# Performance work log

Measured on AMD Instinct MI355X. Metric: run time of the kernel, lower is better.

## Reference

```python
import jax, jax.numpy as jnp
from jax import lax
import numpy as np


def _edt_to(zero_mask):
    """Exact Euclidean distance from every pixel to the nearest True pixel of
    zero_mask. Equivalent to scipy.ndimage.distance_transform_edt(~zero_mask).
    Separable two-pass algorithm: 1-D distance along W (two scans), then an
    exact lower-envelope min along H using squared distances.
    zero_mask: bool [B, H, W] -> float32 [B, H, W].
    """
    B, H, W = zero_mask.shape
    INF = jnp.float32(H + W)  # larger than any attainable 1-D distance
    bg = jnp.transpose(zero_mask, (2, 0, 1))  # [W, B, H]: scan over W

    def step(c, b):
        c = jnp.where(b, 0.0, c + 1.0)
        return c, c

    init = jnp.full((B, H), INF, dtype=jnp.float32)
    _, f = lax.scan(step, init, bg)                 # left-to-right
    _, r = lax.scan(step, init, bg, reverse=True)   # right-to-left
    d1 = jnp.minimum(f, r)                          # [W, B, H] 1-D dist along W
    g = jnp.transpose(d1 * d1, (1, 2, 0))           # [B, H, W] squared 1-D dist

    # d2[b, y, x] = min_{y'} g[b, y', x] + (y - y')^2   (exact 2-D squared EDT)
    yy = jnp.arange(H, dtype=jnp.float32)
    dy2 = (yy[:, None] - yy[None, :]) ** 2          # [H, H']
    d2 = jnp.min(g[:, None, :, :] + dy2[None, :, :, None], axis=2)  # [B, H, W]
    return jnp.sqrt(d2)


def _boundary_loss(preds, targets, idx_class=None):
    B, C, H, W = preds.shape
    probs = jax.nn.softmax(preds, axis=1)
    classes = [idx_class] if idx_class is not None else list(range(1, C))
    total = jnp.float32(0.0)
    count = jnp.float32(0.0)
    for cls in classes:
        pos = targets == cls        # bool [B, H, W]
        neg = ~pos
        has = jnp.any(pos)
        # scipy: distance(negmask)*negmask - (distance(posmask)-1)*posmask
        # distance_transform_edt(negmask) == dist to nearest pos pixel, etc.
        dmap = _edt_to(pos) * neg - (_edt_to(neg) - 1.0) * pos
        loss = jnp.mean(dmap * probs[:, cls])
        total = total + jnp.where(has, loss, 0.0)
        count = count + has.astype(jnp.float32)
    return jnp.where(count > 0, total / jnp.maximum(count, 1.0), jnp.float32(0.0))


def setup_inputs() -> dict:
    key = jax.random.key(0)
    k1, k2 = jax.random.split(key)
    preds = jax.random.normal(k1, (8, 4, 256, 256), dtype=jnp.float32)
    targets = jax.random.randint(k2, (8, 256, 256), 0, 4)
    return {"preds": preds, "targets": targets}


def reference(preds, targets):
    return _boundary_loss(preds, targets, idx_class=None)
```

## Files before the change

kernel.cpp:

```cpp
#include <hip/hip_runtime.h>
#include <math.h>

#define BB 8
#define HH 256
#define WW 256
#define T  2
#define NW 4
#define PAD 96
#define LDSW (WW + 2 * PAD)

typedef unsigned long long u64;

__global__ __launch_bounds__(128) void build_masks(const int* __restrict__ tgt,
                                                   unsigned short* __restrict__ masks16,
                                                   float* __restrict__ out) {
  const int tx = threadIdx.x;
  const int xh = blockIdx.x & 1;
  const int b  = blockIdx.x >> 1;
  const int w  = blockIdx.y;
  const int q  = blockIdx.z;
  const int x  = xh * 128 + tx;
  if (b == 0 && w == 0 && q == 0 && x == 0) out[0] = 0.0f;
  unsigned m0 = 0, m1 = 0, m2 = 0, m3 = 0, bit = 1u;
  const int* p = tgt + ((size_t)b * HH + w * 64 + q * 16) * WW + x;
  for (int r = 0; r < 16; ++r, bit += bit) {
    int e = p[r * WW];
    m0 |= (e == 0) ? bit : 0u;
    m1 |= (e == 1) ? bit : 0u;
    m2 |= (e == 2) ? bit : 0u;
    m3 |= (e == 3) ? bit : 0u;
  }
  unsigned short* mp = masks16 + (((size_t)(b * NW + w) * WW + x) * 4) * 4 + q;
  mp[0]  = (unsigned short)m0;
  mp[4]  = (unsigned short)m1;
  mp[8]  = (unsigned short)m2;
  mp[12] = (unsigned short)m3;
}

__global__ __launch_bounds__(256, 4) void fused(const u64* __restrict__ masks,
                                                const float* __restrict__ preds,
                                                float* __restrict__ out) {
  __shared__ float g[T][LDSW][4];
  __shared__ float fred[4];
  const int x  = threadIdx.x;
  const int b  = blockIdx.x;
  const int y0 = blockIdx.y * T;
  const int wy = y0 >> 6;

  u64 m[NW][4];
  {
    const u64* mb = masks + ((size_t)b * NW * WW + x) * 4;
#pragma unroll
    for (int w = 0; w < NW; ++w) {
      ulonglong2 lo = *(const ulonglong2*)(mb + (size_t)w * WW * 4 + 0);
      ulonglong2 hi = *(const ulonglong2*)(mb + (size_t)w * WW * 4 + 2);
      m[w][0] = lo.x; m[w][1] = lo.y; m[w][2] = hi.x; m[w][3] = hi.y;
    }
  }

  float pr[T][4];
#pragma unroll
  for (int j = 0; j < T; ++j) {
    const float* pb = preds + ((size_t)b * 4 * HH + (y0 + j)) * WW + x;
    pr[j][0] = pb[0 * HH * WW];
    pr[j][1] = pb[1 * HH * WW];
    pr[j][2] = pb[2 * HH * WW];
    pr[j][3] = pb[3 * HH * WW];
  }

  for (int i = x; i < T * 2 * PAD; i += 256) {
    int j = i / (2 * PAD);
    int q = i - j * (2 * PAD);
    int idx = (q < PAD) ? q : (q + WW);
    *(float4*)&g[j][idx][0] = make_float4(1e30f, 1e30f, 1e30f, 1e30f);
  }

  float d[T][4];
  int lmax = 0;
#pragma unroll
  for (int j = 0; j < T; ++j) {
    const int y  = y0 + j;
    const int ly = y & 63;
    const int ini = min(513 + y, 768 - y);
    float4 gv;
    float* gp = (float*)&gv;
#pragma unroll
    for (int k = 0; k < 4; ++k) {
      int best = ini;
#pragma unroll
      for (int w = 0; w < NW; ++w) {
        u64 bits = m[w][k];
        if (w < wy) {
          int dd = y - (w * 64 + 63 - __clzll((long long)bits));
          best = min(best, bits ? dd : 1024);
        } else if (w > wy) {
          int dd = w * 64 + (__ffsll((long long)bits) - 1) - y;
          best = min(best, bits ? dd : 1024);
        } else {
          u64 lo = bits & ((2ull << ly) - 1ull);
          u64 hi = bits >> ly;
          int dl = ly - 63 + __clzll((long long)lo);
          int dh = __ffsll((long long)hi) - 1;
          best = min(best, lo ? dl : 1024);
          best = min(best, hi ? dh : 1024);
        }
      }
      lmax = max(lmax, best);
      gp[k] = (float)(best * best);
      d[j][k] = gp[k];
    }
    *(float4*)&g[j][x + PAD][0] = gv;
  }

#pragma unroll
  for (int off = 32; off; off >>= 1) lmax = max(lmax, __shfl_xor(lmax, off, 64));
  const int R  = __builtin_amdgcn_readfirstlane(lmax);
  const int Rw = min(R, PAD);
  __syncthreads();

  bool alldone = false;
  for (int kk = 1; kk <= Rw; ++kk) {
    float fkk = (float)kk;
    float fk2 = fkk * fkk;
    float dmax = 0.0f;
#pragma unroll
    for (int j = 0; j < T; ++j) {
      float4 gm = *(const float4*)&g[j][x + PAD - kk][0];
      float4 gp = *(const float4*)&g[j][x + PAD + kk][0];
      d[j][0] = fminf(d[j][0], fminf(gm.x, gp.x) + fk2);
      d[j][1] = fminf(d[j][1], fminf(gm.y, gp.y) + fk2);
      d[j][2] = fminf(d[j][2], fminf(gm.z, gp.z) + fk2);
      d[j][3] = fminf(d[j][3], fminf(gm.w, gp.w) + fk2);
      dmax = fmaxf(dmax, fmaxf(fmaxf(d[j][0], d[j][1]), fmaxf(d[j][2], d[j][3])));
    }
    if (__all(dmax <= fk2)) { alldone = true; break; }
  }
  if (!alldone && R > PAD) {
#pragma unroll 1
    for (int kk = PAD + 1; kk <= R; ++kk) {
      int xm = max(x - kk, 0), xp = min(x + kk, WW - 1);
      float dm = (float)(x - xm), dpq = (float)(xp - x);
      float dm2 = dm * dm, dp2 = dpq * dpq;
      float dmax = 0.0f;
#pragma unroll
      for (int j = 0; j < T; ++j) {
        float4 gm = *(const float4*)&g[j][xm + PAD][0];
        float4 gp = *(const float4*)&g[j][xp + PAD][0];
        d[j][0] = fminf(d[j][0], fminf(gm.x + dm2, gp.x + dp2));
        d[j][1] = fminf(d[j][1], fminf(gm.y + dm2, gp.y + dp2));
        d[j][2] = fminf(d[j][2], fminf(gm.z + dm2, gp.z + dp2));
        d[j][3] = fminf(d[j][3], fminf(gm.w + dm2, gp.w + dp2));
        dmax = fmaxf(dmax, fmaxf(fmaxf(d[j][0], d[j][1]), fmaxf(d[j][2], d[j][3])));
      }
      float fkk = (float)kk;
      if (__all(dmax <= fkk * fkk)) break;
    }
  }

  float acc = 0.0f;
#pragma unroll
  for (int j = 0; j < T; ++j) {
    const int ly = (y0 + j) & 63;
    const int t = (int)((m[wy][1] >> ly) & 1ull) * 1 +
                  (int)((m[wy][2] >> ly) & 1ull) * 2 +
                  (int)((m[wy][3] >> ly) & 1ull) * 3;
    float p0 = pr[j][0], p1 = pr[j][1], p2 = pr[j][2], p3 = pr[j][3];
    float pm = fmaxf(fmaxf(p0, p1), fmaxf(p2, p3));
    float e0 = expf(p0 - pm), e1 = expf(p1 - pm);
    float e2 = expf(p2 - pm), e3 = expf(p3 - pm);
    float inv = 1.0f / (e0 + e1 + e2 + e3);

    float dn1 = fminf(d[j][0], fminf(d[j][2], d[j][3]));
    float dn2 = fminf(d[j][0], fminf(d[j][1], d[j][3]));
    float dn3 = fminf(d[j][0], fminf(d[j][1], d[j][2]));
    float c1 = (t == 1) ? (1.0f - sqrtf(dn1)) : sqrtf(d[j][1]);
    float c2 = (t == 2) ? (1.0f - sqrtf(dn2)) : sqrtf(d[j][2]);
    float c3 = (t == 3) ? (1.0f - sqrtf(dn3)) : sqrtf(d[j][3]);
    acc += (c1 * e1 + c2 * e2 + c3 * e3) * inv;
  }

#pragma unroll
  for (int off = 32; off; off >>= 1) acc += __shfl_down(acc, off, 64);
  if ((x & 63) == 0) fred[x >> 6] = acc;
  __syncthreads();
  if (x == 0)
    atomicAdd(out, (fred[0] + fred[1] + fred[2] + fred[3]) *
                       (1.0f / (3.0f * BB * HH * WW)));
}

extern "C" void kernel_launch(void* const* d_in, const int* in_sizes, int n_in,
                              void* d_out, int out_size, void* d_ws, size_t ws_size,
                              hipStream_t stream) {
  const float* preds = (const float*)d_in[0];
  const int*   tgt   = (const int*)d_in[1];
  float* out   = (float*)d_out;
  u64*   masks = (u64*)d_ws;

  build_masks<<<dim3(BB * 2, NW, 4), 128, 0, stream>>>(tgt, (unsigned short*)masks, out);
  fused<<<dim3(BB, HH / T), 256, 0, stream>>>(masks, preds, out);
}
```

Before: 79.76 us.

## Process four rows per block, hoist cross-window column scans, mask finished lanes

Doubles rows per block (T=2→4) and lowers the occupancy hint so each block amortises the mask loads and the per-column scan of the other 64-row windows. The nearest-set-bit positions in the other windows are computed once per column instead of once per row. The horizontal lower-envelope loop now skips the LDS reads for lanes whose current distances are already final, keeping a per-lane done flag. The costs are half as many blocks, higher register and LDS use per block, and extra divergent branches in the inner loop.

```diff
diff --git a/kernel.cpp b/kernel.cpp
--- a/kernel.cpp
+++ b/kernel.cpp
@@ -4,7 +4,7 @@
 #define BB 8
 #define HH 256
 #define WW 256
-#define T  2
+#define T  4
 #define NW 4
 #define PAD 96
 #define LDSW (WW + 2 * PAD)
@@ -37,7 +37,7 @@
   mp[12] = (unsigned short)m3;
 }
 
-__global__ __launch_bounds__(256, 4) void fused(const u64* __restrict__ masks,
+__global__ __launch_bounds__(256, 2) void fused(const u64* __restrict__ masks,
                                                 const float* __restrict__ preds,
                                                 float* __restrict__ out) {
   __shared__ float g[T][LDSW][4];
@@ -75,6 +75,27 @@
     *(float4*)&g[j][idx][0] = make_float4(1e30f, 1e30f, 1e30f, 1e30f);
   }
 
+  int posmax[4] = {-4096, -4096, -4096, -4096};
+  int posmin[4] = { 8192,  8192,  8192,  8192};
+#pragma unroll
+  for (int w = 0; w < NW; ++w) {
+    if (w < wy) {
+#pragma unroll
+      for (int k = 0; k < 4; ++k) {
+        u64 bits = m[w][k];
+        int pos = w * 64 + 63 - __clzll((long long)bits);
+        posmax[k] = max(posmax[k], bits ? pos : -4096);
+      }
+    } else if (w > wy) {
+#pragma unroll
+      for (int k = 0; k < 4; ++k) {
+        u64 bits = m[w][k];
+        int pos = w * 64 + (__ffsll((long long)bits) - 1);
+        posmin[k] = min(posmin[k], bits ? pos : 8192);
+      }
+    }
+  }
+
   float d[T][4];
   int lmax = 0;
 #pragma unroll
@@ -83,31 +104,22 @@
     const int ly = y & 63;
     const int ini = min(513 + y, 768 - y);
     float4 gv;
-    float* gp = (float*)&gv;
+    float* gp_ = (float*)&gv;
 #pragma unroll
     for (int k = 0; k < 4; ++k) {
-      int best = ini;
-#pragma unroll
-      for (int w = 0; w < NW; ++w) {
-        u64 bits = m[w][k];
-        if (w < wy) {
-          int dd = y - (w * 64 + 63 - __clzll((long long)bits));
-          best = min(best, bits ? dd : 1024);
-        } else if (w > wy) {
-          int dd = w * 64 + (__ffsll((long long)bits) - 1) - y;
-          best = min(best, bits ? dd : 1024);
-        } else {
-          u64 lo = bits & ((2ull << ly) - 1ull);
-          u64 hi = bits >> ly;
-          int dl = ly - 63 + __clzll((long long)lo);
-          int dh = __ffsll((long long)hi) - 1;
-          best = min(best, lo ? dl : 1024);
-          best = min(best, hi ? dh : 1024);
-        }
-      }
+      u64 bits = m[wy][k];
+      u64 lo = bits & ((2ull << ly) - 1ull);
+      u64 hi = bits >> ly;
+      int dl = ly - 63 + __clzll((long long)lo);
+      int dh = __ffsll((long long)hi) - 1;
+      int best = min(ini, y - posmax[k]);
+      best = min(best, posmin[k] - y);
+      best = min(best, lo ? dl : 1024);
+      best = min(best, hi ? dh : 1024);
       lmax = max(lmax, best);
-      gp[k] = (float)(best * best);
-      d[j][k] = gp[k];
+      float fb = (float)(best * best);
+      gp_[k] = fb;
+      d[j][k] = fb;
     }
     *(float4*)&g[j][x + PAD][0] = gv;
   }
@@ -118,42 +130,61 @@
   const int Rw = min(R, PAD);
   __syncthreads();
 
+  float mydone = 0.0f;
+#pragma unroll
+  for (int j = 0; j < T; ++j)
+    mydone = fmaxf(mydone,
+                   fmaxf(fmaxf(d[j][0], d[j][1]), fmaxf(d[j][2], d[j][3])));
+
   bool alldone = false;
   for (int kk = 1; kk <= Rw; ++kk) {
     float fkk = (float)kk;
     float fk2 = fkk * fkk;
-    float dmax = 0.0f;
-#pragma unroll
-    for (int j = 0; j < T; ++j) {
-      float4 gm = *(const float4*)&g[j][x + PAD - kk][0];
-      float4 gp = *(const float4*)&g[j][x + PAD + kk][0];
-      d[j][0] = fminf(d[j][0], fminf(gm.x, gp.x) + fk2);
-      d[j][1] = fminf(d[j][1], fminf(gm.y, gp.y) + fk2);
-      d[j][2] = fminf(d[j][2], fminf(gm.z, gp.z) + fk2);
-      d[j][3] = fminf(d[j][3], fminf(gm.w, gp.w) + fk2);
-      dmax = fmaxf(dmax, fmaxf(fmaxf(d[j][0], d[j][1]), fmaxf(d[j][2], d[j][3])));
-    }
-    if (__all(dmax <= fk2)) { alldone = true; break; }
+    bool act = (mydone > fk2);
+    if (__all(!act)) { alldone = true; break; }
+    if (act) {
+#pragma unroll
+      for (int j = 0; j < T; ++j) {
+        float4 gm = *(const float4*)&g[j][x + PAD - kk][0];
+        float4 gq = *(const float4*)&g[j][x + PAD + kk][0];
+        d[j][0] = fminf(d[j][0], fminf(gm.x, gq.x) + fk2);
+        d[j][1] = fminf(d[j][1], fminf(gm.y, gq.y) + fk2);
+        d[j][2] = fminf(d[j][2], fminf(gm.z, gq.z) + fk2);
+        d[j][3] = fminf(d[j][3], fminf(gm.w, gq.w) + fk2);
+      }
+      float md = 0.0f;
+#pragma unroll
+      for (int j = 0; j < T; ++j)
+        md = fmaxf(md, fmaxf(fmaxf(d[j][0], d[j][1]), fmaxf(d[j][2], d[j][3])));
+      mydone = md;
+    }
   }
   if (!alldone && R > PAD) {
 #pragma unroll 1
     for (int kk = PAD + 1; kk <= R; ++kk) {
-      int xm = max(x - kk, 0), xp = min(x + kk, WW - 1);
-      float dm = (float)(x - xm), dpq = (float)(xp - x);
-      float dm2 = dm * dm, dp2 = dpq * dpq;
-      float dmax = 0.0f;
-#pragma unroll
-      for (int j = 0; j < T; ++j) {
-        float4 gm = *(const float4*)&g[j][xm + PAD][0];
-        float4 gp = *(const float4*)&g[j][xp + PAD][0];
-        d[j][0] = fminf(d[j][0], fminf(gm.x + dm2, gp.x + dp2));
-        d[j][1] = fminf(d[j][1], fminf(gm.y + dm2, gp.y + dp2));
-        d[j][2] = fminf(d[j][2], fminf(gm.z + dm2, gp.z + dp2));
-        d[j][3] = fminf(d[j][3], fminf(gm.w + dm2, gp.w + dp2));
-        dmax = fmaxf(dmax, fmaxf(fmaxf(d[j][0], d[j][1]), fmaxf(d[j][2], d[j][3])));
-      }
       float fkk = (float)kk;
-      if (__all(dmax <= fkk * fkk)) break;
+      float fk2 = fkk * fkk;
+      bool act = (mydone > fk2);
+      if (__all(!act)) break;
+      if (act) {
+        int xm = max(x - kk, 0), xp = min(x + kk, WW - 1);
+        float dm = (float)(x - xm), dpq = (float)(xp - x);
+        float dm2 = dm * dm, dp2 = dpq * dpq;
+#pragma unroll
+        for (int j = 0; j < T; ++j) {
+          float4 gm = *(const float4*)&g[j][xm + PAD][0];
+          float4 gq = *(const float4*)&g[j][xp + PAD][0];
+          d[j][0] = fminf(d[j][0], fminf(gm.x + dm2, gq.x + dp2));
+          d[j][1] = fminf(d[j][1], fminf(gm.y + dm2, gq.y + dp2));
+          d[j][2] = fminf(d[j][2], fminf(gm.z + dm2, gq.z + dp2));
+          d[j][3] = fminf(d[j][3], fminf(gm.w + dm2, gq.w + dp2));
+        }
+        float md = 0.0f;
+#pragma unroll
+        for (int j = 0; j < T; ++j)
+          md = fmaxf(md, fmaxf(fmaxf(d[j][0], d[j][1]), fmaxf(d[j][2], d[j][3])));
+        mydone = md;
+      }
     }
   }
 
```

After: 72.72 us (median of 2 runs). 8.8% less time.
